# Kernel tuning notes

Hardware: AMD Instinct MI355X
Metric: run time of the kernel (lower is better)

The kernel has to match this reference:

```python
import jax, jax.numpy as jnp
import numpy as np

N_NODES = 100000
N_EDGES = 1600000
IN_FEATS, N_HIDDEN, N_CLASSES = 128, 64, 40


def setup_inputs() -> dict:
    key = jax.random.key(0)
    ks = jax.random.split(key, 6)
    h = jax.random.normal(ks[0], (N_NODES, IN_FEATS), dtype=jnp.float32)
    W0 = jax.random.normal(ks[1], (IN_FEATS, N_HIDDEN), dtype=jnp.float32) * (1.0 / np.sqrt(IN_FEATS))
    b0 = jnp.zeros((N_HIDDEN,), dtype=jnp.float32)
    W1 = jax.random.normal(ks[2], (N_HIDDEN, N_HIDDEN), dtype=jnp.float32) * (1.0 / np.sqrt(N_HIDDEN))
    b1 = jnp.zeros((N_HIDDEN,), dtype=jnp.float32)
    W2 = jax.random.normal(ks[3], (N_HIDDEN, N_CLASSES), dtype=jnp.float32) * (1.0 / np.sqrt(N_HIDDEN))
    b2 = jnp.zeros((N_CLASSES,), dtype=jnp.float32)
    src = jax.random.randint(ks[4], (N_EDGES,), 0, N_NODES, dtype=jnp.int32)
    dst = jax.random.randint(ks[5], (N_EDGES,), 0, N_NODES, dtype=jnp.int32)
    return {"h": h, "W0": W0, "b0": b0, "W1": W1, "b1": b1, "W2": W2, "b2": b2, "src": src, "dst": dst}


def _degrees(src, dst):
    ones = jnp.ones(src.shape[0], dtype=jnp.float32)
    out_deg = jax.ops.segment_sum(ones, src, num_segments=N_NODES)
    in_deg = jax.ops.segment_sum(ones, dst, num_segments=N_NODES)
    # DGL clamps degrees to >= 1 (allow_zero_in_degree)
    norm_src = jax.lax.rsqrt(jnp.maximum(out_deg, 1.0))  # [N]
    norm_dst = jax.lax.rsqrt(jnp.maximum(in_deg, 1.0))   # [N]
    return norm_src, norm_dst


def _graph_conv(x, W, b, src, dst, norm_src, norm_dst, act):
    # DGL GraphConv, norm='both': D_in^{-1/2} A^T D_out^{-1/2} (X W) + b
    xw = (x @ W) * norm_src[:, None]               # [N, out]
    agg = jax.ops.segment_sum(xw[src], dst, num_segments=N_NODES)  # gather-scatter over edges
    out = agg * norm_dst[:, None] + b
    return jax.nn.relu(out) if act else out


def reference(h, W0, b0, W1, b1, W2, b2, src, dst):
    norm_src, norm_dst = _degrees(src, dst)
    h = _graph_conv(h, W0, b0, src, dst, norm_src, norm_dst, act=True)
    # dropout layers are identity at inference
    h = _graph_conv(h, W1, b1, src, dst, norm_src, norm_dst, act=True)
    h = _graph_conv(h, W2, b2, src, dst, norm_src, norm_dst, act=False)
    return h
```

## Files before the change

### kernel.cpp

```cpp
#include <hip/hip_runtime.h>
#include <hip/hip_fp16.h>

#define N_NODES 100000
#define N_EDGES 1600000
#define ELL_W 64
#define NCHUNK 32
#define NSEG 8
#define CH (N_EDGES / NCHUNK)
#define SEGN (N_NODES / NSEG)

typedef unsigned short ushort4v __attribute__((ext_vector_type(4)));
typedef float float4v __attribute__((ext_vector_type(4)));
typedef _Float16 half8 __attribute__((ext_vector_type(8)));
typedef float floatx4 __attribute__((ext_vector_type(4)));


__global__ __launch_bounds__(512) void k_count(const int* __restrict__ src, const int* __restrict__ dst,
                                               int* __restrict__ cnt_out, int* __restrict__ cnt_in) {
    __shared__ int ci[SEGN];
    __shared__ int co[SEGN];
    const int c = blockIdx.x;
    const int lo = blockIdx.y * SEGN;
    for (int i = threadIdx.x; i < SEGN; i += 512) { ci[i] = 0; co[i] = 0; }
    __syncthreads();
    const int4* s4 = (const int4*)(src + c * CH);
    const int4* d4 = (const int4*)(dst + c * CH);
    for (int i = threadIdx.x; i < CH / 4; i += 512) {
        int4 s = s4[i], d = d4[i];
        unsigned a;
        a = (unsigned)(s.x - lo); if (a < SEGN) atomicAdd(&co[a], 1);
        a = (unsigned)(s.y - lo); if (a < SEGN) atomicAdd(&co[a], 1);
        a = (unsigned)(s.z - lo); if (a < SEGN) atomicAdd(&co[a], 1);
        a = (unsigned)(s.w - lo); if (a < SEGN) atomicAdd(&co[a], 1);
        a = (unsigned)(d.x - lo); if (a < SEGN) atomicAdd(&ci[a], 1);
        a = (unsigned)(d.y - lo); if (a < SEGN) atomicAdd(&ci[a], 1);
        a = (unsigned)(d.z - lo); if (a < SEGN) atomicAdd(&ci[a], 1);
        a = (unsigned)(d.w - lo); if (a < SEGN) atomicAdd(&ci[a], 1);
    }
    __syncthreads();
    for (int i = threadIdx.x; i < SEGN; i += 512) {
        cnt_in [c * N_NODES + lo + i] = ci[i];
        cnt_out[c * N_NODES + lo + i] = co[i];
    }
}

__global__ __launch_bounds__(256) void k_scan(int* __restrict__ cnt_in, const int* __restrict__ cnt_out,
                                              int* __restrict__ fill, float* __restrict__ norm_src,
                                              float* __restrict__ norm_dst) {
    int d = blockIdx.x * 256 + threadIdx.x;
    if (d >= N_NODES) return;
    int run = 0;
    #pragma unroll
    for (int c = 0; c < NCHUNK; ++c) {
        int v = cnt_in[c * N_NODES + d];
        cnt_in[c * N_NODES + d] = run;
        run += v;
    }
    int od = 0;
    #pragma unroll
    for (int c = 0; c < NCHUNK; ++c) od += cnt_out[c * N_NODES + d];
    fill[d] = run;
    norm_dst[d] = rsqrtf((float)(run < 1 ? 1 : run));
    norm_src[d] = rsqrtf((float)(od  < 1 ? 1 : od ));
}

__global__ __launch_bounds__(512) void k_scatter(const int* __restrict__ src, const int* __restrict__ dst,
                                                 const int* __restrict__ bases, int* __restrict__ ell) {
    __shared__ int base[SEGN];
    const int c = blockIdx.x;
    const int lo = blockIdx.y * SEGN;
    for (int i = threadIdx.x; i < SEGN; i += 512) base[i] = bases[c * N_NODES + lo + i];
    __syncthreads();
    const int4* s4 = (const int4*)(src + c * CH);
    const int4* d4 = (const int4*)(dst + c * CH);
    for (int i = threadIdx.x; i < CH / 4; i += 512) {
        int4 s = s4[i], d = d4[i];
        unsigned r; int p;
        r = (unsigned)(d.x - lo); if (r < SEGN) { p = atomicAdd(&base[r], 1); if (p < ELL_W) ell[p * N_NODES + lo + r] = s.x; }
        r = (unsigned)(d.y - lo); if (r < SEGN) { p = atomicAdd(&base[r], 1); if (p < ELL_W) ell[p * N_NODES + lo + r] = s.y; }
        r = (unsigned)(d.z - lo); if (r < SEGN) { p = atomicAdd(&base[r], 1); if (p < ELL_W) ell[p * N_NODES + lo + r] = s.z; }
        r = (unsigned)(d.w - lo); if (r < SEGN) { p = atomicAdd(&base[r], 1); if (p < ELL_W) ell[p * N_NODES + lo + r] = s.w; }
    }
}

template<int K, int NCOL, bool XHALF>
__global__ __launch_bounds__(256) void k_gemm(const void* __restrict__ Xv, const float* __restrict__ W,
                                              const float* __restrict__ norm, __half* __restrict__ Y) {
    constexpr int NT = (NCOL + 15) / 16;
    constexpr int NR = NT * 16;
    __shared__ _Float16 Xh[64][K + 8];
    __shared__ _Float16 Wt[NR][K + 8];
    const int tid = threadIdx.x;
    const int row0 = blockIdx.x * 64;

    for (int idx = tid; idx < K * NCOL; idx += 256) {
        int k = idx / NCOL, c = idx - k * NCOL;
        Wt[c][k] = (_Float16)W[idx];
    }
    if (NCOL != NR) {
        for (int idx = tid; idx < (NR - NCOL) * K; idx += 256) {
            int c = NCOL + idx / K, k = idx - (idx / K) * K;
            Wt[c][k] = (_Float16)0;
        }
    }

    for (int idx = tid; idx < 64 * (K / 8); idx += 256) {
        int r = idx / (K / 8), kc = idx - r * (K / 8);
        int gr = row0 + r;
        half8 v = {0, 0, 0, 0, 0, 0, 0, 0};
        if (gr < N_NODES) {
            if (XHALF) {
                v = *(const half8*)((const _Float16*)Xv + (long)gr * K + kc * 8);
            } else {
                const float* X = (const float*)Xv + (long)gr * K + kc * 8;
                float4 u0 = *(const float4*)(X + 0);
                float4 u1 = *(const float4*)(X + 4);
                v.s0 = (_Float16)u0.x; v.s1 = (_Float16)u0.y;
                v.s2 = (_Float16)u0.z; v.s3 = (_Float16)u0.w;
                v.s4 = (_Float16)u1.x; v.s5 = (_Float16)u1.y;
                v.s6 = (_Float16)u1.z; v.s7 = (_Float16)u1.w;
            }
        }
        *(half8*)&Xh[r][kc * 8] = v;
    }
    __syncthreads();

    const int lane = tid & 63;
    const int wave = tid >> 6;
    const int quad = lane >> 4;
    const int l16 = lane & 15;
    const int r0 = wave * 16;

    floatx4 acc[NT] = {};
    #pragma unroll
    for (int k0 = 0; k0 < K; k0 += 32) {
        half8 a = *(const half8*)&Xh[r0 + l16][k0 + quad * 8];
        #pragma unroll
        for (int t = 0; t < NT; ++t) {
            half8 b = *(const half8*)&Wt[t * 16 + l16][k0 + quad * 8];
            acc[t] = __builtin_amdgcn_mfma_f32_16x16x32_f16(a, b, acc[t], 0, 0, 0);
        }
    }

    #pragma unroll
    for (int i = 0; i < 4; ++i) {
        int gr = row0 + r0 + quad * 4 + i;
        if (gr < N_NODES) {
            float s = norm[gr];
            #pragma unroll
            for (int t = 0; t < NT; ++t) {
                int c = t * 16 + l16;
                if (c < NCOL) Y[(long)gr * NCOL + c] = __float2half(acc[t][i] * s);
            }
        }
    }
}

template<int NF, bool RELU, bool HALF_OUT>
__global__ __launch_bounds__(256) void k_agg(const __half* __restrict__ XW, const int* __restrict__ ell,
                                             const int* __restrict__ deg, const float* __restrict__ norm_dst,
                                             const float* __restrict__ bias, void* __restrict__ OUTv) {
    constexpr int NQ = NF / 8;
    int gid = blockIdx.x * 256 + threadIdx.x;
    int d = gid / NQ;
    int q = gid - d * NQ;
    if (d >= N_NODES) return;
    int dg = deg[d]; if (dg > ELL_W) dg = ELL_W;

    float acc[8] = {};
    int j = 0;
    for (; j + 4 <= dg; j += 4) {
        int i0 = __builtin_nontemporal_load(ell + (j + 0) * N_NODES + d);
        int i1 = __builtin_nontemporal_load(ell + (j + 1) * N_NODES + d);
        int i2 = __builtin_nontemporal_load(ell + (j + 2) * N_NODES + d);
        int i3 = __builtin_nontemporal_load(ell + (j + 3) * N_NODES + d);
        float4 r0 = *(const float4*)(XW + (long)i0 * NF + q * 8);
        float4 r1 = *(const float4*)(XW + (long)i1 * NF + q * 8);
        float4 r2 = *(const float4*)(XW + (long)i2 * NF + q * 8);
        float4 r3 = *(const float4*)(XW + (long)i3 * NF + q * 8);
        const __half2* h0 = (const __half2*)&r0;
        const __half2* h1 = (const __half2*)&r1;
        const __half2* h2 = (const __half2*)&r2;
        const __half2* h3 = (const __half2*)&r3;
        #pragma unroll
        for (int t = 0; t < 4; ++t) {
            float2 f0 = __half22float2(h0[t]);
            float2 f1 = __half22float2(h1[t]);
            float2 f2 = __half22float2(h2[t]);
            float2 f3 = __half22float2(h3[t]);
            acc[2 * t + 0] += (f0.x + f1.x) + (f2.x + f3.x);
            acc[2 * t + 1] += (f0.y + f1.y) + (f2.y + f3.y);
        }
    }
    for (; j < dg; ++j) {
        int s = __builtin_nontemporal_load(ell + j * N_NODES + d);
        float4 r = *(const float4*)(XW + (long)s * NF + q * 8);
        const __half2* hh = (const __half2*)&r;
        #pragma unroll
        for (int t = 0; t < 4; ++t) {
            float2 f = __half22float2(hh[t]);
            acc[2 * t + 0] += f.x;
            acc[2 * t + 1] += f.y;
        }
    }

    float nd = norm_dst[d];
    float o[8];
    #pragma unroll
    for (int t = 0; t < 8; ++t) {
        o[t] = acc[t] * nd + bias[q * 8 + t];
        if (RELU) o[t] = fmaxf(o[t], 0.f);
    }

    if (HALF_OUT) {
        __half* OUT = (__half*)OUTv;
        __half2 p[4];
        #pragma unroll
        for (int t = 0; t < 4; ++t) p[t] = __floats2half2_rn(o[2 * t], o[2 * t + 1]);
        *(float4*)(OUT + (long)d * NF + q * 8) = *(const float4*)p;
    } else {
        float* OUT = (float*)OUTv;
        *(float4*)(OUT + (long)d * NF + q * 8 + 0) = make_float4(o[0], o[1], o[2], o[3]);
        *(float4*)(OUT + (long)d * NF + q * 8 + 4) = make_float4(o[4], o[5], o[6], o[7]);
    }
}

extern "C" void kernel_launch(void* const* d_in, const int* in_sizes, int n_in,
                              void* d_out, int out_size, void* d_ws, size_t ws_size,
                              hipStream_t stream) {
    const float* h  = (const float*)d_in[0];
    const float* W0 = (const float*)d_in[1];
    const float* b0 = (const float*)d_in[2];
    const float* W1 = (const float*)d_in[3];
    const float* b1 = (const float*)d_in[4];
    const float* W2 = (const float*)d_in[5];
    const float* b2 = (const float*)d_in[6];
    const int* src  = (const int*)d_in[7];
    const int* dst  = (const int*)d_in[8];
    float* out = (float*)d_out;

    char* ws = (char*)d_ws;
    size_t off = 0;
    int* fill        = (int*)(ws + off); off += (size_t)N_NODES * 4;
    float* norm_src  = (float*)(ws + off); off += (size_t)N_NODES * 4;
    float* norm_dst  = (float*)(ws + off); off += (size_t)N_NODES * 4;
    int* ell         = (int*)(ws + off); off += (size_t)N_NODES * ELL_W * 4;
    char* big = ws + off;
    int* cnt_in   = (int*)(big);
    int* cnt_out  = (int*)(big + (size_t)NCHUNK * N_NODES * 4);
    __half* bufA  = (__half*)(big);
    __half* bufB  = (__half*)(big + (size_t)NCHUNK * N_NODES * 4);

    k_count<<<dim3(NCHUNK, NSEG), 512, 0, stream>>>(src, dst, cnt_out, cnt_in);
    k_scan<<<(N_NODES + 255) / 256, 256, 0, stream>>>(cnt_in, cnt_out, fill, norm_src, norm_dst);
    k_scatter<<<dim3(NCHUNK, NSEG), 512, 0, stream>>>(src, dst, cnt_in, ell);

    const int gemm_grid = (N_NODES + 63) / 64;

    k_gemm<128, 64, false><<<gemm_grid, 256, 0, stream>>>(h, W0, norm_src, bufA);
    k_agg<64, true, true><<<(N_NODES * 8 + 255) / 256, 256, 0, stream>>>(bufA, ell, fill, norm_dst, b0, bufB);

    k_gemm<64, 64, true><<<gemm_grid, 256, 0, stream>>>(bufB, W1, norm_src, bufA);
    k_agg<64, true, true><<<(N_NODES * 8 + 255) / 256, 256, 0, stream>>>(bufA, ell, fill, norm_dst, b1, bufB);

    k_gemm<64, 40, true><<<gemm_grid, 256, 0, stream>>>(bufB, W2, norm_src, bufA);
    k_agg<40, false, false><<<(N_NODES * 5 + 255) / 256, 256, 0, stream>>>(bufA, ell, fill, norm_dst, b2, out);
}
```

Baseline: 296.7 us.

## Fuse aggregation with next-layer GEMM and shrink count buffers to bytes

Layers 1 and 2 now aggregate neighbour features straight into shared memory and run the next layer's MFMA GEMM in the same kernel. This removes the intermediate half-precision activation write and read plus two launches. The per-chunk degree count arrays are stored as bytes instead of ints, cutting the traffic of the count and scan passes, but this relies on per-chunk counts and prefix sums never exceeding 255. The fused kernel gathers with only 64 rows x 8 quads per block, so gather parallelism per block is lower than in the standalone aggregation.

```diff
diff --git a/kernel.cpp b/kernel.cpp
--- a/kernel.cpp
+++ b/kernel.cpp
@@ -10,13 +10,13 @@
 #define SEGN (N_NODES / NSEG)
 
 typedef unsigned short ushort4v __attribute__((ext_vector_type(4)));
-typedef float float4v __attribute__((ext_vector_type(4)));
 typedef _Float16 half8 __attribute__((ext_vector_type(8)));
 typedef float floatx4 __attribute__((ext_vector_type(4)));
 
 
 __global__ __launch_bounds__(512) void k_count(const int* __restrict__ src, const int* __restrict__ dst,
-                                               int* __restrict__ cnt_out, int* __restrict__ cnt_in) {
+                                               unsigned char* __restrict__ cnt_out,
+                                               unsigned char* __restrict__ cnt_in) {
     __shared__ int ci[SEGN];
     __shared__ int co[SEGN];
     const int c = blockIdx.x;
@@ -39,12 +39,13 @@
     }
     __syncthreads();
     for (int i = threadIdx.x; i < SEGN; i += 512) {
-        cnt_in [c * N_NODES + lo + i] = ci[i];
-        cnt_out[c * N_NODES + lo + i] = co[i];
-    }
-}
-
-__global__ __launch_bounds__(256) void k_scan(int* __restrict__ cnt_in, const int* __restrict__ cnt_out,
+        cnt_in [c * N_NODES + lo + i] = (unsigned char)ci[i];
+        cnt_out[c * N_NODES + lo + i] = (unsigned char)co[i];
+    }
+}
+
+__global__ __launch_bounds__(256) void k_scan(unsigned char* __restrict__ cnt_in,
+                                              const unsigned char* __restrict__ cnt_out,
                                               int* __restrict__ fill, float* __restrict__ norm_src,
                                               float* __restrict__ norm_dst) {
     int d = blockIdx.x * 256 + threadIdx.x;
@@ -53,7 +54,7 @@
     #pragma unroll
     for (int c = 0; c < NCHUNK; ++c) {
         int v = cnt_in[c * N_NODES + d];
-        cnt_in[c * N_NODES + d] = run;
+        cnt_in[c * N_NODES + d] = (unsigned char)run;
         run += v;
     }
     int od = 0;
@@ -65,7 +66,8 @@
 }
 
 __global__ __launch_bounds__(512) void k_scatter(const int* __restrict__ src, const int* __restrict__ dst,
-                                                 const int* __restrict__ bases, int* __restrict__ ell) {
+                                                 const unsigned char* __restrict__ bases,
+                                                 int* __restrict__ ell) {
     __shared__ int base[SEGN];
     const int c = blockIdx.x;
     const int lo = blockIdx.y * SEGN;
@@ -83,43 +85,37 @@
     }
 }
 
-template<int K, int NCOL, bool XHALF>
-__global__ __launch_bounds__(256) void k_gemm(const void* __restrict__ Xv, const float* __restrict__ W,
+template<int K, int NCOL>
+__global__ __launch_bounds__(256) void k_gemm(const float* __restrict__ Xv, const float* __restrict__ W,
                                               const float* __restrict__ norm, __half* __restrict__ Y) {
     constexpr int NT = (NCOL + 15) / 16;
     constexpr int NR = NT * 16;
-    __shared__ _Float16 Xh[64][K + 8];
-    __shared__ _Float16 Wt[NR][K + 8];
+    __shared__ __align__(16) _Float16 Xh[64][K + 8];
+    __shared__ __align__(16) _Float16 Wt[NR][K + 8];
     const int tid = threadIdx.x;
     const int row0 = blockIdx.x * 64;
 
     for (int idx = tid; idx < K * NCOL; idx += 256) {
-        int k = idx / NCOL, c = idx - k * NCOL;
+        int k = idx / NCOL, c = idx - (idx / NCOL) * NCOL;
         Wt[c][k] = (_Float16)W[idx];
     }
-    if (NCOL != NR) {
-        for (int idx = tid; idx < (NR - NCOL) * K; idx += 256) {
-            int c = NCOL + idx / K, k = idx - (idx / K) * K;
-            Wt[c][k] = (_Float16)0;
-        }
+    for (int idx = tid; idx < (NR - NCOL) * K; idx += 256) {
+        int c = NCOL + idx / K, k = idx - (idx / K) * K;
+        Wt[c][k] = (_Float16)0;
     }
 
     for (int idx = tid; idx < 64 * (K / 8); idx += 256) {
-        int r = idx / (K / 8), kc = idx - r * (K / 8);
+        int r = idx / (K / 8), kc = idx - (idx / (K / 8)) * (K / 8);
         int gr = row0 + r;
         half8 v = {0, 0, 0, 0, 0, 0, 0, 0};
         if (gr < N_NODES) {
-            if (XHALF) {
-                v = *(const half8*)((const _Float16*)Xv + (long)gr * K + kc * 8);
-            } else {
-                const float* X = (const float*)Xv + (long)gr * K + kc * 8;
-                float4 u0 = *(const float4*)(X + 0);
-                float4 u1 = *(const float4*)(X + 4);
-                v.s0 = (_Float16)u0.x; v.s1 = (_Float16)u0.y;
-                v.s2 = (_Float16)u0.z; v.s3 = (_Float16)u0.w;
-                v.s4 = (_Float16)u1.x; v.s5 = (_Float16)u1.y;
-                v.s6 = (_Float16)u1.z; v.s7 = (_Float16)u1.w;
-            }
+            const float* X = Xv + (long)gr * K + kc * 8;
+            float4 u0 = *(const float4*)(X + 0);
+            float4 u1 = *(const float4*)(X + 4);
+            v.s0 = (_Float16)u0.x; v.s1 = (_Float16)u0.y;
+            v.s2 = (_Float16)u0.z; v.s3 = (_Float16)u0.w;
+            v.s4 = (_Float16)u1.x; v.s5 = (_Float16)u1.y;
+            v.s6 = (_Float16)u1.z; v.s7 = (_Float16)u1.w;
         }
         *(half8*)&Xh[r][kc * 8] = v;
     }
@@ -156,10 +152,116 @@
     }
 }
 
-template<int NF, bool RELU, bool HALF_OUT>
+template<int K, int NCOL>
+__global__ __launch_bounds__(256) void k_agg_gemm(const __half* __restrict__ XWp, const int* __restrict__ ell,
+                                                  const int* __restrict__ deg, const float* __restrict__ norm_dst,
+                                                  const float* __restrict__ biasp, const float* __restrict__ W,
+                                                  const float* __restrict__ norm, __half* __restrict__ Y) {
+    constexpr int NT = (NCOL + 15) / 16;
+    constexpr int NR = NT * 16;
+    constexpr int NQ = K / 8;
+    __shared__ __align__(16) _Float16 Xh[64][K + 8];
+    __shared__ __align__(16) _Float16 Wt[NR][K + 8];
+    const int tid = threadIdx.x;
+    const int row0 = blockIdx.x * 64;
+
+    for (int idx = tid; idx < K * NCOL; idx += 256) {
+        int k = idx / NCOL, c = idx - (idx / NCOL) * NCOL;
+        Wt[c][k] = (_Float16)W[idx];
+    }
+    for (int idx = tid; idx < (NR - NCOL) * K; idx += 256) {
+        int c = NCOL + idx / K, k = idx - (idx / K) * K;
+        Wt[c][k] = (_Float16)0;
+    }
+
+    for (int item = tid; item < 64 * NQ; item += 256) {
+        int r = item / NQ, q = item - (item / NQ) * NQ;
+        int d = row0 + r;
+        _Float16 res[8] = {};
+        if (d < N_NODES) {
+            int dg = deg[d]; if (dg > ELL_W) dg = ELL_W;
+            float acc[8] = {};
+            int j = 0;
+            for (; j + 4 <= dg; j += 4) {
+                int i0 = __builtin_nontemporal_load(ell + (j + 0) * N_NODES + d);
+                int i1 = __builtin_nontemporal_load(ell + (j + 1) * N_NODES + d);
+                int i2 = __builtin_nontemporal_load(ell + (j + 2) * N_NODES + d);
+                int i3 = __builtin_nontemporal_load(ell + (j + 3) * N_NODES + d);
+                float4 r0v = *(const float4*)(XWp + (long)i0 * K + q * 8);
+                float4 r1v = *(const float4*)(XWp + (long)i1 * K + q * 8);
+                float4 r2v = *(const float4*)(XWp + (long)i2 * K + q * 8);
+                float4 r3v = *(const float4*)(XWp + (long)i3 * K + q * 8);
+                const __half2* h0 = (const __half2*)&r0v;
+                const __half2* h1 = (const __half2*)&r1v;
+                const __half2* h2 = (const __half2*)&r2v;
+                const __half2* h3 = (const __half2*)&r3v;
+                #pragma unroll
+                for (int t = 0; t < 4; ++t) {
+                    float2 f0 = __half22float2(h0[t]);
+                    float2 f1 = __half22float2(h1[t]);
+                    float2 f2 = __half22float2(h2[t]);
+                    float2 f3 = __half22float2(h3[t]);
+                    acc[2 * t + 0] += (f0.x + f1.x) + (f2.x + f3.x);
+                    acc[2 * t + 1] += (f0.y + f1.y) + (f2.y + f3.y);
+                }
+            }
+            for (; j < dg; ++j) {
+                int s = __builtin_nontemporal_load(ell + j * N_NODES + d);
+                float4 rv = *(const float4*)(XWp + (long)s * K + q * 8);
+                const __half2* hh = (const __half2*)&rv;
+                #pragma unroll
+                for (int t = 0; t < 4; ++t) {
+                    float2 f = __half22float2(hh[t]);
+                    acc[2 * t + 0] += f.x;
+                    acc[2 * t + 1] += f.y;
+                }
+            }
+            float nd = norm_dst[d];
+            #pragma unroll
+            for (int t = 0; t < 8; ++t) {
+                float o = acc[t] * nd + biasp[q * 8 + t];
+                res[t] = (_Float16)fmaxf(o, 0.f);
+            }
+        }
+        *(half8*)&Xh[r][q * 8] = *(const half8*)res;
+    }
+    __syncthreads();
+
+    const int lane = tid & 63;
+    const int wave = tid >> 6;
+    const int quad = lane >> 4;
+    const int l16 = lane & 15;
+    const int r0 = wave * 16;
+
+    floatx4 acc[NT] = {};
+    #pragma unroll
+    for (int k0 = 0; k0 < K; k0 += 32) {
+        half8 a = *(const half8*)&Xh[r0 + l16][k0 + quad * 8];
+        #pragma unroll
+        for (int t = 0; t < NT; ++t) {
+            half8 b = *(const half8*)&Wt[t * 16 + l16][k0 + quad * 8];
+            acc[t] = __builtin_amdgcn_mfma_f32_16x16x32_f16(a, b, acc[t], 0, 0, 0);
+        }
+    }
+
+    #pragma unroll
+    for (int i = 0; i < 4; ++i) {
+        int gr = row0 + r0 + quad * 4 + i;
+        if (gr < N_NODES) {
+            float s = norm[gr];
+            #pragma unroll
+            for (int t = 0; t < NT; ++t) {
+                int c = t * 16 + l16;
+                if (c < NCOL) Y[(long)gr * NCOL + c] = __float2half(acc[t][i] * s);
+            }
+        }
+    }
+}
+
+template<int NF>
 __global__ __launch_bounds__(256) void k_agg(const __half* __restrict__ XW, const int* __restrict__ ell,
                                              const int* __restrict__ deg, const float* __restrict__ norm_dst,
-                                             const float* __restrict__ bias, void* __restrict__ OUTv) {
+                                             const float* __restrict__ bias, float* __restrict__ OUT) {
     constexpr int NQ = NF / 8;
     int gid = blockIdx.x * 256 + threadIdx.x;
     int d = gid / NQ;
@@ -207,22 +309,9 @@
     float nd = norm_dst[d];
     float o[8];
     #pragma unroll
-    for (int t = 0; t < 8; ++t) {
-        o[t] = acc[t] * nd + bias[q * 8 + t];
-        if (RELU) o[t] = fmaxf(o[t], 0.f);
-    }
-
-    if (HALF_OUT) {
-        __half* OUT = (__half*)OUTv;
-        __half2 p[4];
-        #pragma unroll
-        for (int t = 0; t < 4; ++t) p[t] = __floats2half2_rn(o[2 * t], o[2 * t + 1]);
-        *(float4*)(OUT + (long)d * NF + q * 8) = *(const float4*)p;
-    } else {
-        float* OUT = (float*)OUTv;
-        *(float4*)(OUT + (long)d * NF + q * 8 + 0) = make_float4(o[0], o[1], o[2], o[3]);
-        *(float4*)(OUT + (long)d * NF + q * 8 + 4) = make_float4(o[4], o[5], o[6], o[7]);
-    }
+    for (int t = 0; t < 8; ++t) o[t] = acc[t] * nd + bias[q * 8 + t];
+    *(float4*)(OUT + (long)d * NF + q * 8 + 0) = make_float4(o[0], o[1], o[2], o[3]);
+    *(float4*)(OUT + (long)d * NF + q * 8 + 4) = make_float4(o[4], o[5], o[6], o[7]);
 }
 
 extern "C" void kernel_launch(void* const* d_in, const int* in_sizes, int n_in,
@@ -245,24 +334,19 @@
     float* norm_src  = (float*)(ws + off); off += (size_t)N_NODES * 4;
     float* norm_dst  = (float*)(ws + off); off += (size_t)N_NODES * 4;
     int* ell         = (int*)(ws + off); off += (size_t)N_NODES * ELL_W * 4;
-    char* big = ws + off;
-    int* cnt_in   = (int*)(big);
-    int* cnt_out  = (int*)(big + (size_t)NCHUNK * N_NODES * 4);
-    __half* bufA  = (__half*)(big);
-    __half* bufB  = (__half*)(big + (size_t)NCHUNK * N_NODES * 4);
+    unsigned char* cnt_in  = (unsigned char*)(ws + off); off += (size_t)NCHUNK * N_NODES;
+    unsigned char* cnt_out = (unsigned char*)(ws + off); off += (size_t)NCHUNK * N_NODES;
+    __half* bufA  = (__half*)(ws + off); off += (size_t)N_NODES * 64 * 2;
+    __half* bufB  = (__half*)(ws + off); off += (size_t)N_NODES * 64 * 2;
 
     k_count<<<dim3(NCHUNK, NSEG), 512, 0, stream>>>(src, dst, cnt_out, cnt_in);
     k_scan<<<(N_NODES + 255) / 256, 256, 0, stream>>>(cnt_in, cnt_out, fill, norm_src, norm_dst);
     k_scatter<<<dim3(NCHUNK, NSEG), 512, 0, stream>>>(src, dst, cnt_in, ell);
 
-    const int gemm_grid = (N_NODES + 63) / 64;
-
-    k_gemm<128, 64, false><<<gemm_grid, 256, 0, stream>>>(h, W0, norm_src, bufA);
-    k_agg<64, true, true><<<(N_NODES * 8 + 255) / 256, 256, 0, stream>>>(bufA, ell, fill, norm_dst, b0, bufB);
-
-    k_gemm<64, 64, true><<<gemm_grid, 256, 0, stream>>>(bufB, W1, norm_src, bufA);
-    k_agg<64, true, true><<<(N_NODES * 8 + 255) / 256, 256, 0, stream>>>(bufA, ell, fill, norm_dst, b1, bufB);
-
-    k_gemm<64, 40, true><<<gemm_grid, 256, 0, stream>>>(bufB, W2, norm_src, bufA);
-    k_agg<40, false, false><<<(N_NODES * 5 + 255) / 256, 256, 0, stream>>>(bufA, ell, fill, norm_dst, b2, out);
-}
+    const int grid = (N_NODES + 63) / 64;
+
+    k_gemm<128, 64><<<grid, 256, 0, stream>>>(h, W0, norm_src, bufA);
+    k_agg_gemm<64, 64><<<grid, 256, 0, stream>>>(bufA, ell, fill, norm_dst, b0, W1, norm_src, bufB);
+    k_agg_gemm<64, 40><<<grid, 256, 0, stream>>>(bufB, ell, fill, norm_dst, b1, W2, norm_src, bufA);
+    k_agg<40><<<(N_NODES * 5 + 255) / 256, 256, 0, stream>>>(bufA, ell, fill, norm_dst, b2, out);
+}
```

Result: faster. 284.2 us (-4.2%).
